# Performance work log

Hardware: AMD Instinct MI355X
Metric: run time of the kernel (lower is better)

The kernel has to match this reference:

```python
import jax, jax.numpy as jnp
import numpy as np

H = 16
D_MODEL = 1024
D_K = D_MODEL // H
SEQ = 4096


def setup_inputs() -> dict:
    key = jax.random.key(0)
    ks = jax.random.split(key, 11)
    s = 1.0 / np.sqrt(D_MODEL)
    inp = {
        "query": jax.random.normal(ks[0], (SEQ, D_MODEL), dtype=jnp.float32),
        "key": jax.random.normal(ks[1], (SEQ, D_MODEL), dtype=jnp.float32),
        "value": jax.random.normal(ks[2], (SEQ, D_MODEL), dtype=jnp.float32),
        "Wq": jax.random.uniform(ks[3], (D_MODEL, D_MODEL), jnp.float32, -s, s),
        "bq": jax.random.uniform(ks[4], (D_MODEL,), jnp.float32, -s, s),
        "Wk": jax.random.uniform(ks[5], (D_MODEL, D_MODEL), jnp.float32, -s, s),
        "bk": jax.random.uniform(ks[6], (D_MODEL,), jnp.float32, -s, s),
        "Wv": jax.random.uniform(ks[7], (D_MODEL, D_MODEL), jnp.float32, -s, s),
        "bv": jax.random.uniform(ks[8], (D_MODEL,), jnp.float32, -s, s),
        "Wo": jax.random.uniform(ks[9], (D_MODEL, D_MODEL), jnp.float32, -s, s),
        "bo": jax.random.uniform(ks[10], (D_MODEL,), jnp.float32, -s, s),
    }
    return inp


def reference(query, key, value, Wq, bq, Wk, bk, Wv, bv, Wo, bo):
    # Linear projections (torch Linear: x @ W.T + b), then split heads.
    # [S, d_model] -> [S, h, d_k] -> [h, S, d_k]
    def proj(x, W, b):
        return (x @ W.T + b).reshape(-1, H, D_K).transpose(1, 0, 2)

    q = proj(query, Wq, bq)   # [h, S, d_k]
    k = proj(key, Wk, bk)     # [h, S, d_k]
    v = proj(value, Wv, bv)   # [h, S, d_k]

    scale = 1.0 / jnp.sqrt(jnp.asarray(D_K, dtype=q.dtype))
    scores = jnp.einsum("hnd,hmd->hnm", q, k) * scale  # [h, S, S]
    p_attn = jax.nn.softmax(scores, axis=-1)
    x = jnp.einsum("hnm,hmd->hnd", p_attn, v)           # [h, S, d_k]
    x = x.transpose(1, 0, 2).reshape(-1, H * D_K)        # [S, d_model]
    return x @ Wo.T + bo
```

## Files before the change

### kernel.cpp

```cpp
#include <hip/hip_runtime.h>
#include <hip/hip_bf16.h>
#include <stdint.h>

#define HN     16
#define DMODEL 1024
#define DKH    64
#define SEQL   4096

typedef __attribute__((ext_vector_type(8))) short bf16x8;
typedef __attribute__((ext_vector_type(4))) float f32x4;

typedef const __attribute__((address_space(1))) uint32_t gas_u32;
typedef __attribute__((address_space(3))) uint32_t las_u32;

__device__ __forceinline__ void gl_lds16(const void* g, void* l) {
  __builtin_amdgcn_global_load_lds((gas_u32*)g, (las_u32*)l, 16, 0, 0);
}

__device__ __forceinline__ unsigned short f2bf(float x) {
  uint32_t u = __float_as_uint(x);
  u = (u + 0x7fffu + ((u >> 16) & 1u)) >> 16;
  return (unsigned short)u;
}

__device__ __forceinline__ uint32_t cvt_pk_bf16(float lo, float hi) {
  uint32_t r;
  asm("v_cvt_pk_bf16_f32 %0, %1, %2" : "=v"(r) : "v"(lo), "v"(hi));
  return r;
}

__device__ __forceinline__ float fast_exp2(float x) {
  float r;
  asm("v_exp_f32 %0, %1" : "=v"(r) : "v"(x));
  return r;
}

struct CvtArgs {
  const float *q, *k, *v, *wq, *wk, *wv, *wo;
  unsigned short *qb, *kb, *vb, *wqb, *wkb, *wvb, *wob;
};

__global__ __launch_bounds__(256) void cvt_all(CvtArgs a) {
  const int stride = gridDim.x * blockDim.x;
  for (int v4 = blockIdx.x * blockDim.x + threadIdx.x; v4 < 4194304; v4 += stride) {
    const float* sp; unsigned short* dp; int idx;
    if      (v4 < 1048576) { sp = a.q;  dp = a.qb;  idx = v4; }
    else if (v4 < 2097152) { sp = a.k;  dp = a.kb;  idx = v4 - 1048576; }
    else if (v4 < 3145728) { sp = a.v;  dp = a.vb;  idx = v4 - 2097152; }
    else if (v4 < 3407872) { sp = a.wq; dp = a.wqb; idx = v4 - 3145728; }
    else if (v4 < 3670016) { sp = a.wk; dp = a.wkb; idx = v4 - 3407872; }
    else if (v4 < 3932160) { sp = a.wv; dp = a.wvb; idx = v4 - 3670016; }
    else                   { sp = a.wo; dp = a.wob; idx = v4 - 3932160; }
    float4 f = ((const float4*)sp)[idx];
    ushort4 o;
    o.x = f2bf(f.x); o.y = f2bf(f.y); o.z = f2bf(f.z); o.w = f2bf(f.w);
    ((ushort4*)dp)[idx] = o;
  }
}

struct GemmDesc {
  const unsigned short* A;
  const unsigned short* W;
  const float* bias;
  void* C;
  int mode;
  float scale;
};
struct GemmArgs { GemmDesc d[3]; };

__global__ __launch_bounds__(256) void gemm_bt(GemmArgs ga) {
  const GemmDesc gd = ga.d[blockIdx.z];
  constexpr int M = SEQL, N = DMODEL, K = DMODEL;
  __shared__ unsigned short As[128 * 64];
  __shared__ unsigned short Bs[128 * 64];
  const int tid = threadIdx.x;
  const int w = tid >> 6, lane = tid & 63;
  const int g16 = lane >> 4, l16 = lane & 15;
  const int wr = w >> 1, wc = w & 1;
  const int bm0 = blockIdx.y * 128, bn0 = blockIdx.x * 128;
  const int srow = tid >> 3, scc = tid & 7;

  f32x4 acc[4][4];
#pragma unroll
  for (int i = 0; i < 4; ++i)
#pragma unroll
    for (int j = 0; j < 4; ++j)
      acc[i][j] = (f32x4){0.f, 0.f, 0.f, 0.f};

  for (int k0 = 0; k0 < K; k0 += 64) {
#pragma unroll
    for (int i = 0; i < 4; ++i) {
      int row = i * 32 + srow;
      int sw = scc ^ (row & 7);
      gl_lds16(gd.A + (size_t)(bm0 + row) * K + k0 + sw * 8,
               (void*)(As + (i * 256 + w * 64) * 8));
      gl_lds16(gd.W + (size_t)(bn0 + row) * K + k0 + sw * 8,
               (void*)(Bs + (i * 256 + w * 64) * 8));
    }
    __syncthreads();
#pragma unroll
    for (int ks = 0; ks < 2; ++ks) {
      bf16x8 af[4], bfr[4];
#pragma unroll
      for (int mt = 0; mt < 4; ++mt) {
        int row = wr * 64 + mt * 16 + l16;
        af[mt] = *(const bf16x8*)&As[row * 64 + (((ks * 4 + g16) ^ (row & 7)) * 8)];
      }
#pragma unroll
      for (int nt = 0; nt < 4; ++nt) {
        int row = wc * 64 + nt * 16 + l16;
        bfr[nt] = *(const bf16x8*)&Bs[row * 64 + (((ks * 4 + g16) ^ (row & 7)) * 8)];
      }
#pragma unroll
      for (int mt = 0; mt < 4; ++mt)
#pragma unroll
        for (int nt = 0; nt < 4; ++nt)
          acc[mt][nt] = __builtin_amdgcn_mfma_f32_16x16x32_bf16(af[mt], bfr[nt], acc[mt][nt], 0, 0, 0);
    }
    __syncthreads();
  }

#pragma unroll
  for (int nt = 0; nt < 4; ++nt) {
    int col = bn0 + wc * 64 + nt * 16 + l16;
    float bcol = gd.bias[col];
#pragma unroll
    for (int mt = 0; mt < 4; ++mt) {
      int row0 = bm0 + wr * 64 + mt * 16 + g16 * 4;
      f32x4 a = acc[mt][nt];
      if (gd.mode == 0) {
        unsigned short* CB = (unsigned short*)gd.C;
#pragma unroll
        for (int r = 0; r < 4; ++r)
          CB[(size_t)(row0 + r) * N + col] = f2bf((a[r] + bcol) * gd.scale);
      } else {
        unsigned short* CT = (unsigned short*)gd.C;
        ushort4 pk;
        pk.x = f2bf(a[0] + bcol); pk.y = f2bf(a[1] + bcol);
        pk.z = f2bf(a[2] + bcol); pk.w = f2bf(a[3] + bcol);
        *(ushort4*)&CT[(size_t)col * M + row0] = pk;
      }
    }
  }
}

__global__ __launch_bounds__(256) void gemm_o(
    const unsigned short* __restrict__ A, const unsigned short* __restrict__ W,
    const float* __restrict__ bias, float* __restrict__ C) {
  constexpr int N = DMODEL, K = DMODEL;
  __shared__ unsigned short As[128 * 64];
  __shared__ unsigned short Bs[64 * 64];
  const int tid = threadIdx.x;
  const int w = tid >> 6, lane = tid & 63;
  const int g16 = lane >> 4, l16 = lane & 15;
  const int wr = w >> 1, wc = w & 1;
  const int bm0 = blockIdx.y * 128, bn0 = blockIdx.x * 64;
  const int srow = tid >> 3, scc = tid & 7;

  f32x4 acc[4][2];
#pragma unroll
  for (int i = 0; i < 4; ++i)
#pragma unroll
    for (int j = 0; j < 2; ++j)
      acc[i][j] = (f32x4){0.f, 0.f, 0.f, 0.f};

  for (int k0 = 0; k0 < K; k0 += 64) {
#pragma unroll
    for (int i = 0; i < 4; ++i) {
      int row = i * 32 + srow;
      int sw = scc ^ (row & 7);
      gl_lds16(A + (size_t)(bm0 + row) * K + k0 + sw * 8,
               (void*)(As + (i * 256 + w * 64) * 8));
    }
#pragma unroll
    for (int i = 0; i < 2; ++i) {
      int row = i * 32 + srow;
      int sw = scc ^ (row & 7);
      gl_lds16(W + (size_t)(bn0 + row) * K + k0 + sw * 8,
               (void*)(Bs + (i * 256 + w * 64) * 8));
    }
    __syncthreads();
#pragma unroll
    for (int ks = 0; ks < 2; ++ks) {
      bf16x8 af[4], bfr[2];
#pragma unroll
      for (int mt = 0; mt < 4; ++mt) {
        int row = wr * 64 + mt * 16 + l16;
        af[mt] = *(const bf16x8*)&As[row * 64 + (((ks * 4 + g16) ^ (row & 7)) * 8)];
      }
#pragma unroll
      for (int nt = 0; nt < 2; ++nt) {
        int row = wc * 32 + nt * 16 + l16;
        bfr[nt] = *(const bf16x8*)&Bs[row * 64 + (((ks * 4 + g16) ^ (row & 7)) * 8)];
      }
#pragma unroll
      for (int mt = 0; mt < 4; ++mt)
#pragma unroll
        for (int nt = 0; nt < 2; ++nt)
          acc[mt][nt] = __builtin_amdgcn_mfma_f32_16x16x32_bf16(af[mt], bfr[nt], acc[mt][nt], 0, 0, 0);
    }
    __syncthreads();
  }

#pragma unroll
  for (int nt = 0; nt < 2; ++nt) {
    int col = bn0 + wc * 32 + nt * 16 + l16;
    float bcol = bias[col];
#pragma unroll
    for (int mt = 0; mt < 4; ++mt) {
      int row0 = bm0 + wr * 64 + mt * 16 + g16 * 4;
#pragma unroll
      for (int r = 0; r < 4; ++r)
        C[(size_t)(row0 + r) * N + col] = acc[mt][nt][r] + bcol;
    }
  }
}

__global__ __launch_bounds__(256, 3) void attn_fwd(
    const unsigned short* __restrict__ Qm, const unsigned short* __restrict__ Km,
    const unsigned short* __restrict__ Vtm, unsigned short* __restrict__ Xm) {
  __shared__ __align__(16) unsigned short Ksm[2 * 4096];
  __shared__ __align__(16) unsigned short Vsm[2 * 4096];
  __shared__ __align__(16) unsigned short Psm[8192];
  const int tid = threadIdx.x;
  const int w = tid >> 6, lane = tid & 63;
  const int g = lane >> 4, qi = lane & 15;
  const int hb = blockIdx.y * DKH;
  const int q0 = blockIdx.x * 128 + w * 32;
  const int srow = tid >> 3, scc = tid & 7;
  const float THR = 12.0f;

  const int r0 = srow, r1 = 32 + srow;
  const unsigned short* kp0 = Km + (size_t)r0 * DMODEL + hb + (scc ^ (r0 & 7)) * 8;
  const unsigned short* kp1 = Km + (size_t)r1 * DMODEL + hb + (scc ^ (r1 & 7)) * 8;
  const unsigned short* vp0 = Vtm + (size_t)(hb + r0) * SEQL + (scc ^ (r0 & 7)) * 8;
  const unsigned short* vp1 = Vtm + (size_t)(hb + r1) * SEQL + (scc ^ (r1 & 7)) * 8;
  unsigned short* kd0 = Ksm + (w * 64) * 8;
  unsigned short* kd1 = Ksm + (256 + w * 64) * 8;
  unsigned short* vd0 = Vsm + (w * 64) * 8;
  unsigned short* vd1 = Vsm + (256 + w * 64) * 8;

  const unsigned short* kb0 = &Ksm[qi * 64 + (((0 + g) ^ (qi & 7)) * 8)];
  const unsigned short* kb1 = &Ksm[qi * 64 + (((4 + g) ^ (qi & 7)) * 8)];
  const unsigned short* vrb0 = &Vsm[qi * 64 + (((0 + g) ^ (qi & 7)) * 8)];
  const unsigned short* vrb1 = &Vsm[qi * 64 + (((4 + g) ^ (qi & 7)) * 8)];

  const int pwb = w * 2048 + qi * 64 + (g & 1) * 4;
  const int pw0 = pwb + (((0 + (g >> 1)) ^ (qi & 7)) * 8);
  const int pw1 = pwb + (((2 + (g >> 1)) ^ (qi & 7)) * 8);
  const int pw2 = pwb + (((4 + (g >> 1)) ^ (qi & 7)) * 8);
  const int pw3 = pwb + (((6 + (g >> 1)) ^ (qi & 7)) * 8);
  const unsigned short* prb0 = &Psm[w * 2048 + qi * 64 + (((0 + g) ^ (qi & 7)) * 8)];
  const unsigned short* prb1 = &Psm[w * 2048 + qi * 64 + (((4 + g) ^ (qi & 7)) * 8)];

  union { uint32_t u[4]; bf16x8 v; } onef;
  onef.u[0] = onef.u[1] = onef.u[2] = onef.u[3] = 0x3F803F80u;

  bf16x8 qf[2][2];
#pragma unroll
  for (int h = 0; h < 2; ++h)
#pragma unroll
    for (int ks = 0; ks < 2; ++ks)
      qf[h][ks] = *(const bf16x8*)&Qm[(size_t)(q0 + h * 16 + qi) * DMODEL + hb + ks * 32 + g * 8];

  f32x4 oacc[2][4];
#pragma unroll
  for (int h = 0; h < 2; ++h)
#pragma unroll
    for (int i = 0; i < 4; ++i) oacc[h][i] = (f32x4){0.f, 0.f, 0.f, 0.f};
  f32x4 lacc[2];
  lacc[0] = lacc[1] = (f32x4){0.f, 0.f, 0.f, 0.f};
  float mrun[2] = {-1e30f, -1e30f};

  gl_lds16(kp0, kd0); gl_lds16(kp1, kd1);
  gl_lds16(vp0, vd0); gl_lds16(vp1, vd1);
  kp0 += 64 * DMODEL; kp1 += 64 * DMODEL; vp0 += 64; vp1 += 64;
  asm volatile("s_waitcnt vmcnt(0)" ::: "memory");
  __builtin_amdgcn_s_barrier();

#define ATTN_STEP(BUF)                                                         \
  do {                                                                         \
    gl_lds16(kp0, kd0 + ((BUF) ^ 1) * 4096);                                   \
    gl_lds16(kp1, kd1 + ((BUF) ^ 1) * 4096);                                   \
    gl_lds16(vp0, vd0 + ((BUF) ^ 1) * 4096);                                   \
    gl_lds16(vp1, vd1 + ((BUF) ^ 1) * 4096);                                   \
    kp0 += 64 * DMODEL; kp1 += 64 * DMODEL; vp0 += 64; vp1 += 64;              \
    f32x4 sv[2][4];                                                            \
    _Pragma("unroll")                                                          \
    for (int h = 0; h < 2; ++h)                                                \
      _Pragma("unroll")                                                        \
      for (int kvt = 0; kvt < 4; ++kvt) sv[h][kvt] = (f32x4){0.f, 0.f, 0.f, 0.f}; \
    __builtin_amdgcn_s_setprio(1);                                             \
    _Pragma("unroll")                                                          \
    for (int kvt = 0; kvt < 4; ++kvt) {                                        \
      bf16x8 ka0 = *(const bf16x8*)(kb0 + (BUF) * 4096 + kvt * 1024);          \
      bf16x8 ka1 = *(const bf16x8*)(kb1 + (BUF) * 4096 + kvt * 1024);          \
      _Pragma("unroll")                                                        \
      for (int h = 0; h < 2; ++h) {                                            \
        sv[h][kvt] = __builtin_amdgcn_mfma_f32_16x16x32_bf16(ka0, qf[h][0], sv[h][kvt], 0, 0, 0); \
        sv[h][kvt] = __builtin_amdgcn_mfma_f32_16x16x32_bf16(ka1, qf[h][1], sv[h][kvt], 0, 0, 0); \
      }                                                                        \
    }                                                                          \
    __builtin_amdgcn_s_setprio(0);                                             \
    float tmax[2];                                                             \
    _Pragma("unroll")                                                          \
    for (int h = 0; h < 2; ++h) {                                              \
      float tm = sv[h][0][0];                                                  \
      _Pragma("unroll")                                                        \
      for (int kvt = 0; kvt < 4; ++kvt)                                        \
        _Pragma("unroll")                                                      \
        for (int r = 0; r < 4; ++r) tm = fmaxf(tm, sv[h][kvt][r]);             \
      tm = fmaxf(tm, __shfl_xor(tm, 16));                                      \
      tm = fmaxf(tm, __shfl_xor(tm, 32));                                      \
      tmax[h] = tm;                                                            \
    }                                                                          \
    float need = fmaxf(tmax[0] - mrun[0], tmax[1] - mrun[1]);                  \
    if (__any(need > THR)) {                                                   \
      _Pragma("unroll")                                                        \
      for (int h = 0; h < 2; ++h) {                                            \
        float mnew = fmaxf(mrun[h], tmax[h]);                                  \
        float alpha = fast_exp2(mrun[h] - mnew);                               \
        _Pragma("unroll")                                                      \
        for (int r = 0; r < 4; ++r) {                                          \
          float ar = __shfl(alpha, (lane & 48) + g * 4 + r);                   \
          lacc[h][r] *= ar;                                                    \
          _Pragma("unroll")                                                    \
          for (int dg = 0; dg < 4; ++dg) oacc[h][dg][r] *= ar;                 \
        }                                                                      \
        mrun[h] = mnew;                                                        \
      }                                                                        \
    }                                                                          \
    _Pragma("unroll")                                                          \
    for (int h = 0; h < 2; ++h) {                                              \
      float p[16];                                                             \
      _Pragma("unroll")                                                        \
      for (int kvt = 0; kvt < 4; ++kvt)                                        \
        _Pragma("unroll")                                                      \
        for (int r = 0; r < 4; ++r)                                            \
          p[kvt * 4 + r] = fast_exp2(sv[h][kvt][r] - mrun[h]);                 \
      uint2 pk;                                                                \
      pk.x = cvt_pk_bf16(p[0], p[1]);  pk.y = cvt_pk_bf16(p[2], p[3]);         \
      *(uint2*)&Psm[pw0 + h * 1024] = pk;                                      \
      pk.x = cvt_pk_bf16(p[4], p[5]);  pk.y = cvt_pk_bf16(p[6], p[7]);         \
      *(uint2*)&Psm[pw1 + h * 1024] = pk;                                      \
      pk.x = cvt_pk_bf16(p[8], p[9]);  pk.y = cvt_pk_bf16(p[10], p[11]);       \
      *(uint2*)&Psm[pw2 + h * 1024] = pk;                                      \
      pk.x = cvt_pk_bf16(p[12], p[13]); pk.y = cvt_pk_bf16(p[14], p[15]);      \
      *(uint2*)&Psm[pw3 + h * 1024] = pk;                                      \
    }                                                                          \
    bf16x8 pa[2][2];                                                           \
    _Pragma("unroll")                                                          \
    for (int h = 0; h < 2; ++h) {                                              \
      pa[h][0] = *(const bf16x8*)(prb0 + h * 1024);                            \
      pa[h][1] = *(const bf16x8*)(prb1 + h * 1024);                            \
    }                                                                          \
    __builtin_amdgcn_s_setprio(1);                                             \
    _Pragma("unroll")                                                          \
    for (int h = 0; h < 2; ++h) {                                              \
      lacc[h] = __builtin_amdgcn_mfma_f32_16x16x32_bf16(pa[h][0], onef.v, lacc[h], 0, 0, 0); \
      lacc[h] = __builtin_amdgcn_mfma_f32_16x16x32_bf16(pa[h][1], onef.v, lacc[h], 0, 0, 0); \
    }                                                                          \
    _Pragma("unroll")                                                          \
    for (int dg = 0; dg < 4; ++dg) {                                           \
      bf16x8 vb0 = *(const bf16x8*)(vrb0 + (BUF) * 4096 + dg * 1024);          \
      bf16x8 vb1 = *(const bf16x8*)(vrb1 + (BUF) * 4096 + dg * 1024);          \
      _Pragma("unroll")                                                        \
      for (int h = 0; h < 2; ++h) {                                            \
        oacc[h][dg] = __builtin_amdgcn_mfma_f32_16x16x32_bf16(pa[h][0], vb0, oacc[h][dg], 0, 0, 0); \
        oacc[h][dg] = __builtin_amdgcn_mfma_f32_16x16x32_bf16(pa[h][1], vb1, oacc[h][dg], 0, 0, 0); \
      }                                                                        \
    }                                                                          \
    __builtin_amdgcn_s_setprio(0);                                             \
    asm volatile("s_waitcnt vmcnt(0)" ::: "memory");                           \
    __builtin_amdgcn_s_barrier();                                              \
  } while (0)

  for (int tt = 0; tt < SEQL / 128; ++tt) {
    ATTN_STEP(0);
    ATTN_STEP(1);
  }
#undef ATTN_STEP

#pragma unroll
  for (int h = 0; h < 2; ++h)
#pragma unroll
    for (int r = 0; r < 4; ++r) {
      float inv = 1.f / lacc[h][r];
      int row = q0 + h * 16 + g * 4 + r;
#pragma unroll
      for (int dg = 0; dg < 4; ++dg)
        Xm[(size_t)row * DMODEL + hb + dg * 16 + qi] = f2bf(oacc[h][dg][r] * inv);
    }
}

extern "C" void kernel_launch(void* const* d_in, const int* in_sizes, int n_in,
                              void* d_out, int out_size, void* d_ws, size_t ws_size,
                              hipStream_t stream) {
  const float* query = (const float*)d_in[0];
  const float* key_  = (const float*)d_in[1];
  const float* value = (const float*)d_in[2];
  const float* Wq = (const float*)d_in[3];
  const float* bq = (const float*)d_in[4];
  const float* Wk = (const float*)d_in[5];
  const float* bk = (const float*)d_in[6];
  const float* Wv = (const float*)d_in[7];
  const float* bv = (const float*)d_in[8];
  const float* Wo = (const float*)d_in[9];
  const float* bo = (const float*)d_in[10];

  char* ws = (char*)d_ws;
  const size_t MB = 1024 * 1024;
  unsigned short* qb  = (unsigned short*)(ws + 0 * MB);
  unsigned short* kb  = (unsigned short*)(ws + 8 * MB);
  unsigned short* vb  = (unsigned short*)(ws + 16 * MB);
  unsigned short* wqb = (unsigned short*)(ws + 24 * MB);
  unsigned short* wkb = (unsigned short*)(ws + 26 * MB);
  unsigned short* wvb = (unsigned short*)(ws + 28 * MB);
  unsigned short* wob = (unsigned short*)(ws + 30 * MB);
  unsigned short* Qp  = (unsigned short*)(ws + 32 * MB);
  unsigned short* Kp  = (unsigned short*)(ws + 40 * MB);
  unsigned short* Vtp = (unsigned short*)(ws + 48 * MB);
  unsigned short* Xp  = (unsigned short*)(ws + 56 * MB);

  CvtArgs ca{query, key_, value, Wq, Wk, Wv, Wo, qb, kb, vb, wqb, wkb, wvb, wob};
  cvt_all<<<dim3(2048), dim3(256), 0, stream>>>(ca);

  const float CE = 0.18033688011112042f;
  GemmArgs gp;
  gp.d[0] = GemmDesc{qb, wqb, bq, (void*)Qp, 0, CE};
  gp.d[1] = GemmDesc{kb, wkb, bk, (void*)Kp, 0, 1.0f};
  gp.d[2] = GemmDesc{vb, wvb, bv, (void*)Vtp, 1, 1.0f};
  gemm_bt<<<dim3(8, 32, 3), dim3(256), 0, stream>>>(gp);

  attn_fwd<<<dim3(SEQL / 128, HN), dim3(256), 0, stream>>>(Qp, Kp, Vtp, Xp);

  gemm_o<<<dim3(16, 32), dim3(256), 0, stream>>>(Xp, wob, bo, (float*)d_out);
}
```

Baseline: 280.1 us.

## Split attention over two KV halves with a separate combine kernel

Splits the attention KV sequence into two halves along a new grid z dimension, so each block handles 2048 keys and writes unnormalized fp32 partial outputs plus row sums and running max to workspace. A new combine kernel merges the two halves with a log-sum-exp rescale and writes the bf16 result. The aim is to double the number of blocks (512 to 1024) and fill the GPU's compute units better. In exchange it adds an extra kernel launch and about 32 MB of fp32 partial writes and reads, and the split path only runs when the workspace is at least 98 MB.

```diff
diff --git a/kernel.cpp b/kernel.cpp
--- a/kernel.cpp
+++ b/kernel.cpp
@@ -216,9 +216,11 @@
   }
 }
 
+template<bool PARTIAL>
 __global__ __launch_bounds__(256, 3) void attn_fwd(
     const unsigned short* __restrict__ Qm, const unsigned short* __restrict__ Km,
-    const unsigned short* __restrict__ Vtm, unsigned short* __restrict__ Xm) {
+    const unsigned short* __restrict__ Vtm, unsigned short* __restrict__ Xm,
+    float* __restrict__ Opart, float* __restrict__ Lbuf) {
   __shared__ __align__(16) unsigned short Ksm[2 * 4096];
   __shared__ __align__(16) unsigned short Vsm[2 * 4096];
   __shared__ __align__(16) unsigned short Psm[8192];
@@ -227,14 +229,16 @@
   const int g = lane >> 4, qi = lane & 15;
   const int hb = blockIdx.y * DKH;
   const int q0 = blockIdx.x * 128 + w * 32;
+  const int kv0 = PARTIAL ? blockIdx.z * 2048 : 0;
+  const int NKV = PARTIAL ? 32 : 64;
   const int srow = tid >> 3, scc = tid & 7;
   const float THR = 12.0f;
 
   const int r0 = srow, r1 = 32 + srow;
-  const unsigned short* kp0 = Km + (size_t)r0 * DMODEL + hb + (scc ^ (r0 & 7)) * 8;
-  const unsigned short* kp1 = Km + (size_t)r1 * DMODEL + hb + (scc ^ (r1 & 7)) * 8;
-  const unsigned short* vp0 = Vtm + (size_t)(hb + r0) * SEQL + (scc ^ (r0 & 7)) * 8;
-  const unsigned short* vp1 = Vtm + (size_t)(hb + r1) * SEQL + (scc ^ (r1 & 7)) * 8;
+  const unsigned short* kp0 = Km + (size_t)(kv0 + r0) * DMODEL + hb + (scc ^ (r0 & 7)) * 8;
+  const unsigned short* kp1 = Km + (size_t)(kv0 + r1) * DMODEL + hb + (scc ^ (r1 & 7)) * 8;
+  const unsigned short* vp0 = Vtm + (size_t)(hb + r0) * SEQL + kv0 + (scc ^ (r0 & 7)) * 8;
+  const unsigned short* vp1 = Vtm + (size_t)(hb + r1) * SEQL + kv0 + (scc ^ (r1 & 7)) * 8;
   unsigned short* kd0 = Ksm + (w * 64) * 8;
   unsigned short* kd1 = Ksm + (256 + w * 64) * 8;
   unsigned short* vd0 = Vsm + (w * 64) * 8;
@@ -375,22 +379,63 @@
     __builtin_amdgcn_s_barrier();                                              \
   } while (0)
 
-  for (int tt = 0; tt < SEQL / 128; ++tt) {
+  for (int tt = 0; tt < NKV / 2; ++tt) {
     ATTN_STEP(0);
     ATTN_STEP(1);
   }
 #undef ATTN_STEP
 
-#pragma unroll
-  for (int h = 0; h < 2; ++h)
-#pragma unroll
-    for (int r = 0; r < 4; ++r) {
-      float inv = 1.f / lacc[h][r];
-      int row = q0 + h * 16 + g * 4 + r;
-#pragma unroll
-      for (int dg = 0; dg < 4; ++dg)
-        Xm[(size_t)row * DMODEL + hb + dg * 16 + qi] = f2bf(oacc[h][dg][r] * inv);
-    }
+  if constexpr (PARTIAL) {
+    float* Op = Opart + (size_t)blockIdx.z * (SEQL * DMODEL);
+    float* Lp = Lbuf + (size_t)blockIdx.z * (SEQL * HN * 2);
+#pragma unroll
+    for (int h = 0; h < 2; ++h)
+#pragma unroll
+      for (int r = 0; r < 4; ++r) {
+        int row = q0 + h * 16 + g * 4 + r;
+        float msh = __shfl(mrun[h], (lane & 48) + g * 4 + r);
+#pragma unroll
+        for (int dg = 0; dg < 4; ++dg)
+          Op[(size_t)row * DMODEL + hb + dg * 16 + qi] = oacc[h][dg][r];
+        if (qi == 0) {
+          Lp[(row * HN + blockIdx.y) * 2]     = lacc[h][r];
+          Lp[(row * HN + blockIdx.y) * 2 + 1] = msh;
+        }
+      }
+  } else {
+#pragma unroll
+    for (int h = 0; h < 2; ++h)
+#pragma unroll
+      for (int r = 0; r < 4; ++r) {
+        float inv = 1.f / lacc[h][r];
+        int row = q0 + h * 16 + g * 4 + r;
+#pragma unroll
+        for (int dg = 0; dg < 4; ++dg)
+          Xm[(size_t)row * DMODEL + hb + dg * 16 + qi] = f2bf(oacc[h][dg][r] * inv);
+      }
+  }
+}
+
+__global__ __launch_bounds__(256) void attn_combine(
+    const float* __restrict__ Opart, const float* __restrict__ Lbuf,
+    unsigned short* __restrict__ Xm) {
+  const int idx4 = blockIdx.x * 256 + threadIdx.x;
+  const int row = idx4 >> 8;
+  const int col = (idx4 & 255) * 4;
+  const int head = col >> 6;
+  float2 lm0 = ((const float2*)Lbuf)[row * HN + head];
+  float2 lm1 = ((const float2*)(Lbuf + SEQL * HN * 2))[row * HN + head];
+  float m = fmaxf(lm0.y, lm1.y);
+  float w0 = fast_exp2(lm0.y - m), w1 = fast_exp2(lm1.y - m);
+  float inv = 1.f / (lm0.x * w0 + lm1.x * w1);
+  float4 o0 = *(const float4*)&Opart[(size_t)row * DMODEL + col];
+  float4 o1 = *(const float4*)&Opart[(size_t)SEQL * DMODEL + (size_t)row * DMODEL + col];
+  ushort4 res;
+  res.x = f2bf((o0.x * w0 + o1.x * w1) * inv);
+  res.y = f2bf((o0.y * w0 + o1.y * w1) * inv);
+  res.z = f2bf((o0.z * w0 + o1.z * w1) * inv);
+  res.w = f2bf((o0.w * w0 + o1.w * w1) * inv);
+  *(ushort4*)&Xm[(size_t)row * DMODEL + col] = res;
 }
 
 extern "C" void kernel_launch(void* const* d_in, const int* in_sizes, int n_in,
@@ -421,6 +466,8 @@
   unsigned short* Kp  = (unsigned short*)(ws + 40 * MB);
   unsigned short* Vtp = (unsigned short*)(ws + 48 * MB);
   unsigned short* Xp  = (unsigned short*)(ws + 56 * MB);
+  float* Opart = (float*)(ws + 64 * MB);
+  float* Lbuf  = (float*)(ws + 96 * MB);
 
   CvtArgs ca{query, key_, value, Wq, Wk, Wv, Wo, qb, kb, vb, wqb, wkb, wvb, wob};
   cvt_all<<<dim3(2048), dim3(256), 0, stream>>>(ca);
@@ -432,7 +479,14 @@
   gp.d[2] = GemmDesc{vb, wvb, bv, (void*)Vtp, 1, 1.0f};
   gemm_bt<<<dim3(8, 32, 3), dim3(256), 0, stream>>>(gp);
 
-  attn_fwd<<<dim3(SEQL / 128, HN), dim3(256), 0, stream>>>(Qp, Kp, Vtp, Xp);
+  if (ws_size >= 98 * MB) {
+    attn_fwd<true><<<dim3(SEQL / 128, HN, 2), dim3(256), 0, stream>>>(
+        Qp, Kp, Vtp, nullptr, Opart, Lbuf);
+    attn_combine<<<dim3(4096), dim3(256), 0, stream>>>(Opart, Lbuf, Xp);
+  } else {
+    attn_fwd<false><<<dim3(SEQL / 128, HN, 1), dim3(256), 0, stream>>>(
+        Qp, Kp, Vtp, Xp, nullptr, nullptr);
+  }
 
   gemm_o<<<dim3(16, 32), dim3(256), 0, stream>>>(Xp, wob, bo, (float*)d_out);
 }
```

New measurement: 284.1 us. No clear change (+1.4%).
